# Optimization experiments

Measured on AMD Instinct MI355X. Metric: run time of the kernel, lower is better.

Reference implementation:

```python
import jax, jax.numpy as jnp
import numpy as np

B, NB, NA, D, PF = 16384, 8, 16, 128, 1
IN_DIM = D + NA * D + D  # basis + flattened sf + task = 2304
QK_DIM = D * 3 * PF      # 384
V_DIM = D * PF           # 128


def rbf_similarity(x, y):
    # RBF kernel over the feature axis: exp(-0.5 * ||x - y||^2)
    return jnp.exp(-0.5 * jnp.sum((x - y) ** 2, axis=-1))


def setup_inputs() -> dict:
    key = jax.random.key(0)
    ks = jax.random.split(key, 9)
    basis = jax.random.normal(ks[0], (B, NB, D), dtype=jnp.float32)
    sf_all = jax.random.normal(ks[1], (B, NB, NA, D), dtype=jnp.float32)
    task = jax.random.normal(ks[2], (B, NB, D), dtype=jnp.float32)
    mask = (jax.random.uniform(ks[3], (B, NB, D * PF)) > 0.5).astype(jnp.float32)
    s_in = 1.0 / np.sqrt(IN_DIM)
    s_v = 1.0 / np.sqrt(D)
    Wq = jax.random.normal(ks[4], (IN_DIM, QK_DIM), dtype=jnp.float32) * s_in
    Wk = jax.random.normal(ks[5], (IN_DIM, QK_DIM), dtype=jnp.float32) * s_in
    bk = jnp.zeros((QK_DIM,), dtype=jnp.float32)
    Wv = jax.random.normal(ks[6], (D, V_DIM), dtype=jnp.float32) * s_v
    bv = jnp.zeros((V_DIM,), dtype=jnp.float32)
    return {"basis_features_all": basis, "sf_all": sf_all, "task": task, "mask": mask,
            "Wq": Wq, "Wk": Wk, "bk": bk, "Wv": Wv, "bv": bv}


def reference(basis_features_all, sf_all, task, mask, Wq, Wk, bk, Wv, bv):
    b = sf_all.shape[0]
    sf_all_r = jnp.reshape(sf_all, (b, NB, NA * D))          # (B, NB, NA*D)
    sf_first_r = sf_all_r[:, :1, :]                          # (B, 1, NA*D)
    task = jax.lax.stop_gradient(task)
    task_n = task / jnp.linalg.norm(task, ord=2, axis=-1, keepdims=True)

    # RBF similarity side-branch between consecutive beakers
    bst = jnp.concatenate([basis_features_all, sf_all_r, task_n], axis=-1)  # (B, NB, IN_DIM)
    sim = rbf_similarity(bst[:, :-1, :], bst[:, 1:, :]).mean(axis=0)        # (NB-1,)

    bf_first = basis_features_all[:, :1, :]
    bf_rest = jax.lax.stop_gradient(basis_features_all[:, 1:, :])
    bf_all = jnp.concatenate([bf_first, bf_rest], axis=1)

    q_in = jnp.concatenate([bf_first, sf_first_r, task_n[:, :1, :]], axis=-1)  # (B, 1, IN_DIM)
    query = q_in @ Wq                                                          # (B, 1, QK)
    k_in = jnp.concatenate([bf_all, sf_all_r, task_n], axis=-1)                # (B, NB, IN_DIM)
    keys = k_in @ Wk + bk                                                      # (B, NB, QK)
    values = sf_all @ Wv + bv                                                  # (B, NB, NA, V)

    mask_rep = jnp.repeat(mask, 3, axis=-1)                                    # (B, NB, QK)
    keys_masked = keys * mask_rep
    values_masked = values

    attn_logits = jnp.matmul(query, jnp.swapaxes(keys_masked, -2, -1)) / jnp.sqrt(jnp.float32(D * PF))
    attn_logits = jnp.where(attn_logits == 0, -1e9, attn_logits)               # zero-mask trick
    attention_weights = jax.nn.softmax(attn_logits, axis=-1)                   # (B, 1, NB)

    attended_sf = jnp.einsum('bna,baqf->bnqf', attention_weights, values_masked)  # (B, 1, NA, V)
    task_first = task[:, 0, :]                                                    # (B, D)
    q_1 = jnp.einsum('bi,bnji->bj', task_first, attended_sf)                      # (B, NA)
    return (q_1, attended_sf, attn_logits, attention_weights, keys_masked, values_masked, sim)
```

## Files before the change

kernel.cpp:

```cpp
#include <hip/hip_runtime.h>
#include <hip/hip_bf16.h>
#include <math.h>

static constexpr size_t OFF_ATT = 262144;
static constexpr size_t OFF_LOG = 33816576;
static constexpr size_t OFF_W   = 33947648;
static constexpr size_t OFF_KM  = 34078720;
static constexpr size_t OFF_VM  = 84410368;
static constexpr size_t OFF_SIM = 352845824;

typedef short bf16x8 __attribute__((ext_vector_type(8)));
typedef float f32x4 __attribute__((ext_vector_type(4)));

__device__ inline unsigned short f2bf(float f) {
  union { float f; unsigned u; } x; x.f = f;
  unsigned r = x.u + 0x7FFFu + ((x.u >> 16) & 1u);
  return (unsigned short)(r >> 16);
}

__device__ inline float wave_sum(float v) {
#pragma unroll
  for (int o = 32; o > 0; o >>= 1) v += __shfl_xor(v, o, 64);
  return v;
}

__global__ void norm_kernel(const float* __restrict__ task, float* __restrict__ invn,
                            float* __restrict__ simo) {
  int idx = blockIdx.x * 4 + (threadIdx.x >> 6);
  int lane = threadIdx.x & 63;
  float t0 = task[(size_t)idx * 128 + lane];
  float t1 = task[(size_t)idx * 128 + 64 + lane];
  float s = wave_sum(t0 * t0 + t1 * t1);
  if (lane == 0) invn[idx] = rsqrtf(s);
  if (blockIdx.x == 0 && threadIdx.x < 7) simo[threadIdx.x] = 0.0f;
}

__global__ void wprep_t(const float* __restrict__ W, unsigned short* __restrict__ WT,
                        int K, int N) {
  int ntn = N >> 6;
  int kt = blockIdx.x / ntn, nt = blockIdx.x % ntn;
  int k0 = kt * 64, n0 = nt * 64;
  __shared__ float t[64][65];
  int tid = threadIdx.x;
  int r = tid >> 2, c0 = (tid & 3) * 16;
#pragma unroll
  for (int q = 0; q < 4; ++q) {
    float4 v = *(const float4*)(W + (size_t)(k0 + r) * N + n0 + c0 + q * 4);
    t[r][c0 + q * 4 + 0] = v.x; t[r][c0 + q * 4 + 1] = v.y;
    t[r][c0 + q * 4 + 2] = v.z; t[r][c0 + q * 4 + 3] = v.w;
  }
  __syncthreads();
  int n = tid >> 2, kc0 = (tid & 3) * 16;
#pragma unroll
  for (int q = 0; q < 4; ++q) {
    int kc = kc0 + q * 4;
    ushort4 o = make_ushort4(f2bf(t[kc + 0][n]), f2bf(t[kc + 1][n]),
                             f2bf(t[kc + 2][n]), f2bf(t[kc + 3][n]));
    *(ushort4*)(WT + (size_t)(n0 + n) * K + k0 + kc) = o;
  }
}

__global__ __launch_bounds__(576) void abuild_sim(const float* __restrict__ basis,
                                                  const float* __restrict__ sf,
                                                  const float* __restrict__ task,
                                                  const float* __restrict__ invn,
                                                  unsigned short* __restrict__ Abf,
                                                  float* __restrict__ simo) {
  int b = blockIdx.x;
  int f = threadIdx.x;
  size_t row0 = (size_t)b * 8;
  float4 v[8];
#pragma unroll
  for (int n = 0; n < 8; ++n) {
    size_t row = row0 + n;
    float4 x;
    if (f < 32)       x = *(const float4*)(basis + row * 128 + f * 4);
    else if (f < 544) x = *(const float4*)(sf + row * 2048 + (f - 32) * 4);
    else {
      x = *(const float4*)(task + row * 128 + (f - 544) * 4);
      float s = invn[row];
      x.x *= s; x.y *= s; x.z *= s; x.w *= s;
    }
    v[n] = x;
    ushort4 o = make_ushort4(f2bf(x.x), f2bf(x.y), f2bf(x.z), f2bf(x.w));
    *(ushort4*)(Abf + row * 2304 + f * 4) = o;
  }
  float s7[7];
#pragma unroll
  for (int n = 1; n < 8; ++n) {
    float dx = v[n].x - v[n - 1].x, dy = v[n].y - v[n - 1].y;
    float dz = v[n].z - v[n - 1].z, dw = v[n].w - v[n - 1].w;
    s7[n - 1] = dx * dx + dy * dy + dz * dz + dw * dw;
  }
  __shared__ float red[9][7];
  int wid = threadIdx.x >> 6, lane = threadIdx.x & 63;
#pragma unroll
  for (int i = 0; i < 7; ++i) {
    float p = wave_sum(s7[i]);
    if (lane == 0) red[wid][i] = p;
  }
  __syncthreads();
  if (threadIdx.x < 7) {
    float s = 0.f;
#pragma unroll
    for (int w = 0; w < 9; ++w) s += red[w][threadIdx.x];
    atomicAdd(&simo[threadIdx.x], expf(-0.5f * s) * (1.0f / 16384.0f));
  }
}

template <int MODE>
__global__ __launch_bounds__(256) void qk_gemm(const unsigned short* __restrict__ Abf,
                                               const unsigned short* __restrict__ WT,
                                               const float* __restrict__ bias,
                                               const float* __restrict__ mask,
                                               float* __restrict__ outp) {
  __shared__ unsigned short As[2 * 4096];
  __shared__ unsigned short Bs[2 * 4096];
  int nwg = gridDim.x, per = nwg >> 3;
  int bid = blockIdx.x;
  int swz = (bid & 7) * per + (bid >> 3);
  int mt = swz / 3, nt = swz - mt * 3;
  int tid = threadIdx.x;
  int wave = tid >> 6, lane = tid & 63;
  int wr = wave >> 1, wc = wave & 1;
  int m0g = mt * 128, n0g = nt * 128;

  int c_lo = wave * 2 * 64 + lane;
  int row_q0 = c_lo >> 2, kc_q0 = (c_lo & 3) * 8;
  int c_hi = c_lo + 64;
  int row_q1 = c_hi >> 2, kc_q1 = (c_hi & 3) * 8;
  size_t ga_q0 = (MODE == 1) ? (size_t)(m0g + row_q0) * 8 : (size_t)(m0g + row_q0);
  size_t ga_q1 = (MODE == 1) ? (size_t)(m0g + row_q1) * 8 : (size_t)(m0g + row_q1);
  const unsigned short* ag0 = Abf + ga_q0 * 2304 + kc_q0;
  const unsigned short* ag1 = Abf + ga_q1 * 2304 + kc_q1;
  const unsigned short* bg0 = WT + (size_t)(n0g + row_q0) * 2304 + kc_q0;
  const unsigned short* bg1 = WT + (size_t)(n0g + row_q1) * 2304 + kc_q1;
  int ldsoff0 = wave * 2 * 512;
  int ldsoff1 = ldsoff0 + 512;

#define STAGE(ks, cur)                                                                   \
  do {                                                                                   \
    int _k0 = (ks) * 32;                                                                 \
    unsigned short* _a = As + (cur) * 4096;                                              \
    unsigned short* _b = Bs + (cur) * 4096;                                              \
    __builtin_amdgcn_global_load_lds(                                                    \
        (const __attribute__((address_space(1))) void*)(ag0 + _k0),                      \
        (__attribute__((address_space(3))) void*)(_a + ldsoff0), 16, 0, 0);              \
    __builtin_amdgcn_global_load_lds(                                                    \
        (const __attribute__((address_space(1))) void*)(ag1 + _k0),                      \
        (__attribute__((address_space(3))) void*)(_a + ldsoff1), 16, 0, 0);              \
    __builtin_amdgcn_global_load_lds(                                                    \
        (const __attribute__((address_space(1))) void*)(bg0 + _k0),                      \
        (__attribute__((address_space(3))) void*)(_b + ldsoff0), 16, 0, 0);              \
    __builtin_amdgcn_global_load_lds(                                                    \
        (const __attribute__((address_space(1))) void*)(bg1 + _k0),                      \
        (__attribute__((address_space(3))) void*)(_b + ldsoff1), 16, 0, 0);              \
  } while (0)

  f32x4 acc[4][4];
#pragma unroll
  for (int i = 0; i < 4; ++i)
#pragma unroll
    for (int j = 0; j < 4; ++j) acc[i][j] = (f32x4)(0.f);

  int la = lane & 15, lk = (lane >> 4) * 8;

  STAGE(0, 0);
  __syncthreads();
  int cur = 0;
  for (int ks = 0; ks < 72; ++ks) {
    if (ks < 71) STAGE(ks + 1, cur ^ 1);
    const unsigned short* aL = As + cur * 4096;
    const unsigned short* bL = Bs + cur * 4096;
    bf16x8 af[4], bf[4];
#pragma unroll
    for (int mi = 0; mi < 4; ++mi)
      af[mi] = *(const bf16x8*)(aL + (wr * 64 + mi * 16 + la) * 32 + lk);
#pragma unroll
    for (int ni = 0; ni < 4; ++ni)
      bf[ni] = *(const bf16x8*)(bL + (wc * 64 + ni * 16 + la) * 32 + lk);
#pragma unroll
    for (int mi = 0; mi < 4; ++mi)
#pragma unroll
      for (int ni = 0; ni < 4; ++ni)
        acc[mi][ni] = __builtin_amdgcn_mfma_f32_16x16x32_bf16(af[mi], bf[ni], acc[mi][ni], 0, 0, 0);
    __syncthreads();
    cur ^= 1;
  }
#undef STAGE

  int rq = lane >> 4;
#pragma unroll
  for (int mi = 0; mi < 4; ++mi) {
#pragma unroll
    for (int ni = 0; ni < 4; ++ni) {
      int colg = nt * 128 + wc * 64 + ni * 16 + la;
#pragma unroll
      for (int j = 0; j < 4; ++j) {
        int rowg = mt * 128 + wr * 64 + mi * 16 + rq * 4 + j;
        float v = acc[mi][ni][j];
        if (MODE == 0)
          v = (v + bias[colg]) * mask[(size_t)rowg * 128 + (unsigned)colg / 3u];
        outp[(size_t)rowg * 384 + colg] = v;
      }
    }
  }
}

__global__ __launch_bounds__(256) void attn_kernel4(const float* __restrict__ query,
                                                    const float* __restrict__ km,
                                                    float* __restrict__ logits,
                                                    float* __restrict__ wts) {
  int w = threadIdx.x >> 6, lane = threadIdx.x & 63;
  int b = blockIdx.x * 4 + w;
  float q[6];
#pragma unroll
  for (int j = 0; j < 6; ++j) q[j] = query[(size_t)b * 384 + lane + 64 * j];
  float lg[8];
#pragma unroll
  for (int n = 0; n < 8; ++n) {
    const float* kr = km + ((size_t)b * 8 + n) * 384;
    float p = 0.f;
#pragma unroll
    for (int j = 0; j < 6; ++j) p = fmaf(q[j], kr[lane + 64 * j], p);
    p = wave_sum(p);
    float l = p * 0.08838834764831845f;
    lg[n] = (l == 0.0f) ? -1e9f : l;
  }
  float m = lg[0];
#pragma unroll
  for (int i = 1; i < 8; ++i) m = fmaxf(m, lg[i]);
  float ex[8], s = 0.f;
#pragma unroll
  for (int i = 0; i < 8; ++i) { ex[i] = expf(lg[i] - m); s += ex[i]; }
  float inv = 1.0f / s;
  if (lane < 8) {
    float lv = lg[0], ev = ex[0];
#pragma unroll
    for (int i = 1; i < 8; ++i)
      if (lane == i) { lv = lg[i]; ev = ex[i]; }
    logits[(size_t)b * 8 + lane] = lv;
    wts[(size_t)b * 8 + lane] = ev * inv;
  }
}

template <int ABF>
__global__ __launch_bounds__(256) void v_gemm_attend(const float* __restrict__ sf,
                                                     const unsigned short* __restrict__ Abf,
                                                     const float* __restrict__ Wv,
                                                     const unsigned short* __restrict__ WvT,
                                                     const float* __restrict__ bv,
                                                     const float* __restrict__ wts,
                                                     const float* __restrict__ task,
                                                     float* __restrict__ vm,
                                                     float* __restrict__ att,
                                                     float* __restrict__ q1) {
  __shared__ unsigned short As[128 * 40];
  __shared__ unsigned short Bs[128 * 136];
  float* attL = (float*)As;
  int bid = blockIdx.x;
  int swz = (bid & 7) * 2048 + (bid >> 3);
  int b = swz;
  size_t m0 = (size_t)swz * 128;
  int tid = threadIdx.x;
  int wave = tid >> 6, lane = tid & 63;
  int wr = wave >> 1, wc = wave & 1;
  int r = tid >> 1, h = tid & 1;
  int la = lane & 15, lkq = lane >> 4;

  if (ABF) {
#pragma unroll
    for (int q = 0; q < 8; ++q) {
      bf16x8 v = *(const bf16x8*)(WvT + (size_t)r * 128 + h * 64 + q * 8);
      *(bf16x8*)(Bs + r * 136 + h * 64 + q * 8) = v;
    }
  } else {
#pragma unroll
    for (int q = 0; q < 16; ++q) {
      int flat = q * 256 + tid;
      int k = flat >> 5;
      int n4 = (flat & 31) * 4;
      float4 v = *(const float4*)(Wv + (size_t)k * 128 + n4);
      Bs[(n4 + 0) * 136 + k] = f2bf(v.x);
      Bs[(n4 + 1) * 136 + k] = f2bf(v.y);
      Bs[(n4 + 2) * 136 + k] = f2bf(v.z);
      Bs[(n4 + 3) * 136 + k] = f2bf(v.w);
    }
  }

  const unsigned short* abase = nullptr;
  if (ABF) {
    int n = r >> 4, a = r & 15;
    abase = Abf + ((size_t)b * 8 + n) * 2304 + 128 + (size_t)a * 128 + h * 16;
  }

  f32x4 acc[4][4];
#pragma unroll
  for (int i = 0; i < 4; ++i)
#pragma unroll
    for (int j = 0; j < 4; ++j) acc[i][j] = (f32x4)(0.f);

  for (int ks = 0; ks < 4; ++ks) {
    int k0 = ks * 32;
    if (ABF) {
      bf16x8 u0 = *(const bf16x8*)(abase + k0);
      bf16x8 u1 = *(const bf16x8*)(abase + k0 + 8);
      *(bf16x8*)(As + r * 40 + h * 16)     = u0;
      *(bf16x8*)(As + r * 40 + h * 16 + 8) = u1;
    } else {
      const float* ap = sf + (m0 + r) * 128 + k0 + h * 16;
      float4 v0 = *(const float4*)(ap);
      float4 v1 = *(const float4*)(ap + 4);
      float4 v2 = *(const float4*)(ap + 8);
      float4 v3 = *(const float4*)(ap + 12);
      ushort4 p0 = make_ushort4(f2bf(v0.x), f2bf(v0.y), f2bf(v0.z), f2bf(v0.w));
      ushort4 p1 = make_ushort4(f2bf(v1.x), f2bf(v1.y), f2bf(v1.z), f2bf(v1.w));
      ushort4 p2 = make_ushort4(f2bf(v2.x), f2bf(v2.y), f2bf(v2.z), f2bf(v2.w));
      ushort4 p3 = make_ushort4(f2bf(v3.x), f2bf(v3.y), f2bf(v3.z), f2bf(v3.w));
      *(ushort4*)(As + r * 40 + h * 16)      = p0;
      *(ushort4*)(As + r * 40 + h * 16 + 4)  = p1;
      *(ushort4*)(As + r * 40 + h * 16 + 8)  = p2;
      *(ushort4*)(As + r * 40 + h * 16 + 12) = p3;
    }
    __syncthreads();
    bf16x8 af[4], bfr[4];
#pragma unroll
    for (int mi = 0; mi < 4; ++mi)
      af[mi] = *(const bf16x8*)(As + (wr * 64 + mi * 16 + la) * 40 + lkq * 8);
#pragma unroll
    for (int ni = 0; ni < 4; ++ni)
      bfr[ni] = *(const bf16x8*)(Bs + (wc * 64 + ni * 16 + la) * 136 + k0 + lkq * 8);
#pragma unroll
    for (int mi = 0; mi < 4; ++mi)
#pragma unroll
      for (int ni = 0; ni < 4; ++ni)
        acc[mi][ni] = __builtin_amdgcn_mfma_f32_16x16x32_bf16(af[mi], bfr[ni], acc[mi][ni], 0, 0, 0);
    __syncthreads();
  }

  float w4[4];
#pragma unroll
  for (int mi = 0; mi < 4; ++mi) w4[mi] = wts[(size_t)b * 8 + wr * 4 + mi];
  float pacc[4][4];
#pragma unroll
  for (int ni = 0; ni < 4; ++ni)
#pragma unroll
    for (int j = 0; j < 4; ++j) pacc[ni][j] = 0.f;
#pragma unroll
  for (int mi = 0; mi < 4; ++mi) {
#pragma unroll
    for (int ni = 0; ni < 4; ++ni) {
      int colg = wc * 64 + ni * 16 + la;
      float bb = bv[colg];
#pragma unroll
      for (int j = 0; j < 4; ++j) {
        size_t rowg = m0 + wr * 64 + mi * 16 + lkq * 4 + j;
        float v = acc[mi][ni][j] + bb;
        vm[rowg * 128 + colg] = v;
        pacc[ni][j] = fmaf(w4[mi], v, pacc[ni][j]);
      }
    }
  }
  if (wr == 0) {
#pragma unroll
    for (int ni = 0; ni < 4; ++ni)
#pragma unroll
      for (int j = 0; j < 4; ++j)
        attL[(lkq * 4 + j) * 132 + wc * 64 + ni * 16 + la] = pacc[ni][j];
  }
  __syncthreads();
  if (wr == 1) {
#pragma unroll
    for (int ni = 0; ni < 4; ++ni)
#pragma unroll
      for (int j = 0; j < 4; ++j)
        attL[(lkq * 4 + j) * 132 + wc * 64 + ni * 16 + la] += pacc[ni][j];
  }
  __syncthreads();
#pragma unroll
  for (int i = 0; i < 2; ++i) {
    int fidx = tid + i * 256;
    int a = fidx >> 5, c = (fidx & 31) * 4;
    f32x4 vv = *(const f32x4*)(attL + a * 132 + c);
    *(f32x4*)(att + (size_t)b * 2048 + a * 128 + c) = vv;
  }
  for (int j = wave; j < 16; j += 4) {
    float p = task[(size_t)b * 1024 + lane] * attL[j * 132 + lane]
            + task[(size_t)b * 1024 + 64 + lane] * attL[j * 132 + 64 + lane];
    p = wave_sum(p);
    if (lane == 0) q1[(size_t)b * 16 + j] = p;
  }
}

extern "C" void kernel_launch(void* const* d_in, const int* in_sizes, int n_in,
                              void* d_out, int out_size, void* d_ws, size_t ws_size,
                              hipStream_t stream) {
  const float* basis = (const float*)d_in[0];
  const float* sf    = (const float*)d_in[1];
  const float* task  = (const float*)d_in[2];
  const float* mask  = (const float*)d_in[3];
  const float* Wq    = (const float*)d_in[4];
  const float* Wk    = (const float*)d_in[5];
  const float* bk    = (const float*)d_in[6];
  const float* Wv    = (const float*)d_in[7];
  const float* bv    = (const float*)d_in[8];

  float* out  = (float*)d_out;
  float* q1   = out;
  float* att  = out + OFF_ATT;
  float* logi = out + OFF_LOG;
  float* wts  = out + OFF_W;
  float* km   = out + OFF_KM;
  float* vm   = out + OFF_VM;
  float* simo = out + OFF_SIM;

  constexpr size_t WS_NEED = 603979776ull + 1769472ull + 1769472ull + 32768ull +
                             25165824ull + 524288ull;
  bool usews = ws_size >= WS_NEED;

  unsigned short *Abf, *WkT, *WqT, *WvT = nullptr;
  float *query, *invn;
  if (usews) {
    unsigned char* ws = (unsigned char*)d_ws;
    Abf   = (unsigned short*)ws;
    WkT   = (unsigned short*)(ws + 603979776ull);
    WqT   = (unsigned short*)(ws + 605749248ull);
    WvT   = (unsigned short*)(ws + 607518720ull);
    query = (float*)(ws + 607551488ull);
    invn  = (float*)(ws + 632717312ull);
  } else {
    query = att;
    invn  = att + 6291456;
    WkT   = (unsigned short*)(att + 6422528);
    WqT   = WkT + 884736;
    Abf   = (unsigned short*)vm;
  }

  norm_kernel<<<32768, 256, 0, stream>>>(task, invn, simo);
  wprep_t<<<216, 256, 0, stream>>>(Wk, WkT, 2304, 384);
  wprep_t<<<216, 256, 0, stream>>>(Wq, WqT, 2304, 384);
  if (usews) wprep_t<<<4, 256, 0, stream>>>(Wv, WvT, 128, 128);
  abuild_sim<<<16384, 576, 0, stream>>>(basis, sf, task, invn, Abf, simo);
  qk_gemm<0><<<3072, 256, 0, stream>>>(Abf, WkT, bk, mask, km);
  qk_gemm<1><<<384, 256, 0, stream>>>(Abf, WqT, nullptr, nullptr, query);
  attn_kernel4<<<4096, 256, 0, stream>>>(query, km, logi, wts);
  if (usews)
    v_gemm_attend<1><<<16384, 256, 0, stream>>>(sf, Abf, Wv, WvT, bv, wts, task, vm, att, q1);
  else
    v_gemm_attend<0><<<16384, 256, 0, stream>>>(sf, Abf, Wv, WvT, bv, wts, task, vm, att, q1);
}
```

Baseline: 1.310 ms.

## XOR-swizzle LDS tiles and double-buffer V GEMM A loads via direct-to-LDS

Applies an XOR swizzle to the 16-byte chunk index of the LDS A/B tiles in the QK GEMM, so MFMA fragment reads from rows with a 64-byte stride no longer collide on the same banks. In the bf16 path of the V GEMM, the A tile is now staged with global_load_lds into a double-buffered, swizzled LDS layout instead of register load/store, and the next k-step is prefetched while the current one computes. The goal is fewer LDS bank conflicts and overlap of global loads with MFMA work, at the cost of more LDS for the A buffer in the V kernel, which may lower occupancy.

```diff
diff --git a/kernel.cpp b/kernel.cpp
--- a/kernel.cpp
+++ b/kernel.cpp
@@ -125,17 +125,17 @@
   int wr = wave >> 1, wc = wave & 1;
   int m0g = mt * 128, n0g = nt * 128;
 
-  int c_lo = wave * 2 * 64 + lane;
-  int row_q0 = c_lo >> 2, kc_q0 = (c_lo & 3) * 8;
+  int c_lo = wave * 128 + lane;
+  int row_q0 = c_lo >> 2, kc_q0 = ((c_lo & 3) ^ ((row_q0 >> 1) & 3)) * 8;
   int c_hi = c_lo + 64;
-  int row_q1 = c_hi >> 2, kc_q1 = (c_hi & 3) * 8;
+  int row_q1 = c_hi >> 2, kc_q1 = ((c_hi & 3) ^ ((row_q1 >> 1) & 3)) * 8;
   size_t ga_q0 = (MODE == 1) ? (size_t)(m0g + row_q0) * 8 : (size_t)(m0g + row_q0);
   size_t ga_q1 = (MODE == 1) ? (size_t)(m0g + row_q1) * 8 : (size_t)(m0g + row_q1);
   const unsigned short* ag0 = Abf + ga_q0 * 2304 + kc_q0;
   const unsigned short* ag1 = Abf + ga_q1 * 2304 + kc_q1;
   const unsigned short* bg0 = WT + (size_t)(n0g + row_q0) * 2304 + kc_q0;
   const unsigned short* bg1 = WT + (size_t)(n0g + row_q1) * 2304 + kc_q1;
-  int ldsoff0 = wave * 2 * 512;
+  int ldsoff0 = wave * 1024;
   int ldsoff1 = ldsoff0 + 512;
 
 #define STAGE(ks, cur)                                                                   \
@@ -163,7 +163,8 @@
 #pragma unroll
     for (int j = 0; j < 4; ++j) acc[i][j] = (f32x4)(0.f);
 
-  int la = lane & 15, lk = (lane >> 4) * 8;
+  int la = lane & 15;
+  int sl = (((lane >> 4) ^ ((la >> 1) & 3))) * 8;
 
   STAGE(0, 0);
   __syncthreads();
@@ -175,10 +176,10 @@
     bf16x8 af[4], bf[4];
 #pragma unroll
     for (int mi = 0; mi < 4; ++mi)
-      af[mi] = *(const bf16x8*)(aL + (wr * 64 + mi * 16 + la) * 32 + lk);
+      af[mi] = *(const bf16x8*)(aL + (wr * 64 + mi * 16 + la) * 32 + sl);
 #pragma unroll
     for (int ni = 0; ni < 4; ++ni)
-      bf[ni] = *(const bf16x8*)(bL + (wc * 64 + ni * 16 + la) * 32 + lk);
+      bf[ni] = *(const bf16x8*)(bL + (wc * 64 + ni * 16 + la) * 32 + sl);
 #pragma unroll
     for (int mi = 0; mi < 4; ++mi)
 #pragma unroll
@@ -255,7 +256,7 @@
                                                      float* __restrict__ vm,
                                                      float* __restrict__ att,
                                                      float* __restrict__ q1) {
-  __shared__ unsigned short As[128 * 40];
+  __shared__ unsigned short As[2 * 4096];
   __shared__ unsigned short Bs[128 * 136];
   float* attL = (float*)As;
   int bid = blockIdx.x;
@@ -267,6 +268,7 @@
   int wr = wave >> 1, wc = wave & 1;
   int r = tid >> 1, h = tid & 1;
   int la = lane & 15, lkq = lane >> 4;
+  int sl = ((lkq ^ ((la >> 1) & 3))) * 8;
 
   if (ABF) {
 #pragma unroll
@@ -288,10 +290,21 @@
     }
   }
 
-  const unsigned short* abase = nullptr;
+  const unsigned short *ap0 = nullptr, *ap1 = nullptr;
+  int ldsA0 = wave * 1024, ldsA1 = ldsA0 + 512;
   if (ABF) {
-    int n = r >> 4, a = r & 15;
-    abase = Abf + ((size_t)b * 8 + n) * 2304 + 128 + (size_t)a * 128 + h * 16;
+    int p0 = wave * 128 + lane;
+    int tr0 = p0 >> 2, ds0 = (p0 & 3) ^ ((tr0 >> 1) & 3);
+    int p1 = p0 + 64;
+    int tr1 = p1 >> 2, ds1 = (p1 & 3) ^ ((tr1 >> 1) & 3);
+    ap0 = Abf + ((size_t)b * 8 + (tr0 >> 4)) * 2304 + 128 + (tr0 & 15) * 128 + ds0 * 8;
+    ap1 = Abf + ((size_t)b * 8 + (tr1 >> 4)) * 2304 + 128 + (tr1 & 15) * 128 + ds1 * 8;
+    __builtin_amdgcn_global_load_lds(
+        (const __attribute__((address_space(1))) void*)(ap0),
+        (__attribute__((address_space(3))) void*)(As + ldsA0), 16, 0, 0);
+    __builtin_amdgcn_global_load_lds(
+        (const __attribute__((address_space(1))) void*)(ap1),
+        (__attribute__((address_space(3))) void*)(As + ldsA1), 16, 0, 0);
   }
 
   f32x4 acc[4][4];
@@ -300,13 +313,20 @@
 #pragma unroll
     for (int j = 0; j < 4; ++j) acc[i][j] = (f32x4)(0.f);
 
+  if (ABF) __syncthreads();
+
+  int cur = 0;
   for (int ks = 0; ks < 4; ++ks) {
     int k0 = ks * 32;
     if (ABF) {
-      bf16x8 u0 = *(const bf16x8*)(abase + k0);
-      bf16x8 u1 = *(const bf16x8*)(abase + k0 + 8);
-      *(bf16x8*)(As + r * 40 + h * 16)     = u0;
-      *(bf16x8*)(As + r * 40 + h * 16 + 8) = u1;
+      if (ks < 3) {
+        __builtin_amdgcn_global_load_lds(
+            (const __attribute__((address_space(1))) void*)(ap0 + k0 + 32),
+            (__attribute__((address_space(3))) void*)(As + (cur ^ 1) * 4096 + ldsA0), 16, 0, 0);
+        __builtin_amdgcn_global_load_lds(
+            (const __attribute__((address_space(1))) void*)(ap1 + k0 + 32),
+            (__attribute__((address_space(3))) void*)(As + (cur ^ 1) * 4096 + ldsA1), 16, 0, 0);
+      }
     } else {
       const float* ap = sf + (m0 + r) * 128 + k0 + h * 16;
       float4 v0 = *(const float4*)(ap);
@@ -321,12 +341,16 @@
       *(ushort4*)(As + r * 40 + h * 16 + 4)  = p1;
       *(ushort4*)(As + r * 40 + h * 16 + 8)  = p2;
       *(ushort4*)(As + r * 40 + h * 16 + 12) = p3;
-    }
-    __syncthreads();
+      __syncthreads();
+    }
+    const unsigned short* aL = ABF ? (As + cur * 4096) : As;
     bf16x8 af[4], bfr[4];
 #pragma unroll
-    for (int mi = 0; mi < 4; ++mi)
-      af[mi] = *(const bf16x8*)(As + (wr * 64 + mi * 16 + la) * 40 + lkq * 8);
+    for (int mi = 0; mi < 4; ++mi) {
+      int rowl = wr * 64 + mi * 16 + la;
+      af[mi] = ABF ? *(const bf16x8*)(aL + rowl * 32 + sl)
+                   : *(const bf16x8*)(aL + rowl * 40 + lkq * 8);
+    }
 #pragma unroll
     for (int ni = 0; ni < 4; ++ni)
       bfr[ni] = *(const bf16x8*)(Bs + (wc * 64 + ni * 16 + la) * 136 + k0 + lkq * 8);
@@ -336,6 +360,7 @@
       for (int ni = 0; ni < 4; ++ni)
         acc[mi][ni] = __builtin_amdgcn_mfma_f32_16x16x32_bf16(af[mi], bfr[ni], acc[mi][ni], 0, 0, 0);
     __syncthreads();
+    cur ^= 1;
   }
 
   float w4[4];
```

After: 1.283 ms. 2.1% less time.
